# Kernel tuning notes

Hardware: AMD Instinct MI355X
Metric: run time of the kernel (lower is better)

## Reference

```python
import jax, jax.numpy as jnp
import numpy as np

SCALING = 32.0 / 16.0  # alpha / r

def setup_inputs() -> dict:
    key = jax.random.key(0)
    k1, k2, k3, k4 = jax.random.split(key, 4)
    B_, S, D_in, D_out, R = 4, 2048, 4096, 4096, 16
    x = jax.random.normal(k1, (B_, S, D_in), dtype=jnp.float32)
    W_base = jax.random.normal(k2, (D_out, D_in), dtype=jnp.float32) * 0.02
    b_base = jax.random.normal(k3, (D_out,), dtype=jnp.float32) * 0.02
    A = jax.random.normal(k4, (R, D_in), dtype=jnp.float32) * 0.02
    B = jnp.zeros((D_out, R), dtype=jnp.float32)  # lora_B init to zeros
    return {"x": x, "W_base": W_base, "b_base": b_base, "A": A, "B": B}

def reference(x, W_base, b_base, A, B):
    # base linear (stands in for dequantized 4-bit matmul): [B,S,Din] @ [Din,Dout]
    out = jnp.einsum('bsd,od->bso', x, W_base) + b_base
    # LoRA path: B(A(x)) * scaling, dropout=0 -> identity
    xa = jnp.einsum('bsd,rd->bsr', x, A)        # [B,S,r]
    delta = jnp.einsum('bsr,or->bso', xa, B)    # [B,S,Dout]
    return out + delta * SCALING
```

## Files before the change

### kernel.cpp

```cpp
#include <hip/hip_runtime.h>


typedef __attribute__((ext_vector_type(4))) float f32x4;
typedef __attribute__((ext_vector_type(8))) short bf16x8;

__device__ __forceinline__ unsigned short f2bf(float f) {
    unsigned u = __builtin_bit_cast(unsigned, f);
    unsigned r = u + 0x7fffu + ((u >> 16) & 1u);
    return (unsigned short)(r >> 16);
}

__device__ __forceinline__ void gload_lds16(const void* g, void* l) {
    __builtin_amdgcn_global_load_lds(
        (const __attribute__((address_space(1))) void*)g,
        (__attribute__((address_space(3))) void*)l, 16, 0, 0);
}

__global__ __launch_bounds__(256) void cast_x_kernel(
    const float* __restrict__ x, unsigned short* __restrict__ xb, int n8)
{
    int stride = gridDim.x * blockDim.x;
    for (int i = blockIdx.x * blockDim.x + threadIdx.x; i < n8; i += stride) {
        size_t base = (size_t)i * 8;
        float4 f0 = *(const float4*)&x[base];
        float4 f1 = *(const float4*)&x[base + 4];
        ushort4 o0, o1;
        o0.x = f2bf(f0.x); o0.y = f2bf(f0.y); o0.z = f2bf(f0.z); o0.w = f2bf(f0.w);
        o1.x = f2bf(f1.x); o1.y = f2bf(f1.y); o1.z = f2bf(f1.z); o1.w = f2bf(f1.w);
        *(ushort4*)&xb[base]     = o0;
        *(ushort4*)&xb[base + 4] = o1;
    }
}

__global__ __launch_bounds__(256) void prep_w_kernel(
    const float* __restrict__ W, const float* __restrict__ A,
    const float* __restrict__ Bl, unsigned short* __restrict__ wb,
    int K, float scale)
{
    __shared__ float Bs[16][16];
    const int t = threadIdx.x;
    const int n0 = blockIdx.y * 16;
    const int k0 = blockIdx.x * 256;
    {
        int nl = t >> 4, r = t & 15;
        Bs[nl][r] = Bl[(size_t)(n0 + nl) * 16 + r];
    }
    __syncthreads();

    const int lane = t & 63;
    const int wv = t >> 6;
    const int k = k0 + lane * 4;

    float4 av[16];
#pragma unroll
    for (int r = 0; r < 16; ++r)
        av[r] = *(const float4*)&A[(size_t)r * K + k];

#pragma unroll
    for (int j = 0; j < 4; ++j) {
        const int nl = wv * 4 + j;
        const int n = n0 + nl;
        float4 w = *(const float4*)&W[(size_t)n * K + k];
        float d0 = 0.f, d1 = 0.f, d2 = 0.f, d3 = 0.f;
#pragma unroll
        for (int r = 0; r < 16; ++r) {
            float b = Bs[nl][r];
            d0 += b * av[r].x; d1 += b * av[r].y;
            d2 += b * av[r].z; d3 += b * av[r].w;
        }
        ushort4 o;
        o.x = f2bf(w.x + scale * d0);
        o.y = f2bf(w.y + scale * d1);
        o.z = f2bf(w.z + scale * d2);
        o.w = f2bf(w.w + scale * d3);
        *(ushort4*)&wb[(size_t)n * K + k] = o;
    }
}


#define SETPRIO(p) __builtin_amdgcn_s_setprio(p)
#define BARRIER()  __builtin_amdgcn_s_barrier()
#define LGKM(n)    asm volatile("s_waitcnt lgkmcnt(" #n ")" ::: "memory")

__global__ __launch_bounds__(512, 2) void gemm256_kernel(
    const unsigned short* __restrict__ Xb, const unsigned short* __restrict__ Wb,
    const float* __restrict__ bias, float* __restrict__ out,
    int M, int N, int K)
{
    __shared__ __align__(16) unsigned short lds[2][2][2][8192];

    const int NT = K / 64;
    const int ntn = N / 256;
    int bid = blockIdx.x;
    {
        int per = gridDim.x >> 3;
        bid = (bid & 7) * per + (bid >> 3);
    }
    const int tm = bid / ntn, tn = bid % ntn;

    const int t = threadIdx.x;
    const int lane = t & 63, wave = t >> 6;
    const int wr = wave >> 2;
    const int wc = wave & 3;
    const int wch = wc >> 1;
    const int bro = (wc & 1) * 64;

    const int srow = t >> 3;
    const int scol = ((t & 7) * 8) ^ (((t >> 3) & 7) << 3);
    unsigned gA[2][2], gB[2][2];
#pragma unroll
    for (int h = 0; h < 2; ++h)
#pragma unroll
        for (int i = 0; i < 2; ++i) {
            gA[h][i] = (unsigned)((tm * 256 + h * 128 + i * 64 + srow) * K + scol);
            gB[h][i] = (unsigned)((tn * 256 + h * 128 + i * 64 + srow) * K + scol);
        }

#define ST_A4(buf, ktt)                                                         \
    _Pragma("unroll") for (int h = 0; h < 2; ++h)                               \
    _Pragma("unroll") for (int i = 0; i < 2; ++i)                               \
        gload_lds16(Xb + gA[h][i] + (ktt) * 64,                                 \
                    &lds[buf][0][h][i * 4096 + wave * 512]);
#define ST_B4(buf, ktt)                                                         \
    _Pragma("unroll") for (int h = 0; h < 2; ++h)                               \
    _Pragma("unroll") for (int i = 0; i < 2; ++i)                               \
        gload_lds16(Wb + gB[h][i] + (ktt) * 64,                                 \
                    &lds[buf][1][h][i * 4096 + wave * 512]);

    const int fr = lane & 15;
    const int hi16 = ((lane >> 4) & 3) * 16;
    const int bsw = (fr & 7) << 4;
    const int lo0 = hi16 ^ bsw;
    const int lo1 = (64 + hi16) ^ bsw;

    f32x4 acc[8][4] = {};
    bf16x8 a03[4][2], a47[4][2], b01[2][2], b23[2][2];

#define RD_A03(P)                                                               \
    _Pragma("unroll") for (int i = 0; i < 4; ++i) {                             \
        a03[i][0] = *(const bf16x8*)((P) + (i * 16 + fr) * 128 + lo0);          \
        a03[i][1] = *(const bf16x8*)((P) + (i * 16 + fr) * 128 + lo1);          \
    }
#define RD_A47(P)                                                               \
    _Pragma("unroll") for (int i = 0; i < 4; ++i) {                             \
        a47[i][0] = *(const bf16x8*)((P) + ((4 + i) * 16 + fr) * 128 + lo0);    \
        a47[i][1] = *(const bf16x8*)((P) + ((4 + i) * 16 + fr) * 128 + lo1);    \
    }
#define RD_B01(P)                                                               \
    _Pragma("unroll") for (int i = 0; i < 2; ++i) {                             \
        b01[i][0] = *(const bf16x8*)((P) + (bro + i * 16 + fr) * 128 + lo0);    \
        b01[i][1] = *(const bf16x8*)((P) + (bro + i * 16 + fr) * 128 + lo1);    \
    }
#define RD_B23(P)                                                               \
    _Pragma("unroll") for (int i = 0; i < 2; ++i) {                             \
        b23[i][0] = *(const bf16x8*)((P) + (bro + (2+i) * 16 + fr) * 128 + lo0);\
        b23[i][1] = *(const bf16x8*)((P) + (bro + (2+i) * 16 + fr) * 128 + lo1);\
    }

#define MFMA_Q(AV, BV, M0, N0)                                                  \
    _Pragma("unroll") for (int mi = 0; mi < 4; ++mi)                            \
    _Pragma("unroll") for (int ni = 0; ni < 2; ++ni)                            \
    _Pragma("unroll") for (int kk = 0; kk < 2; ++kk)                            \
        acc[(M0) + mi][(N0) + ni] = __builtin_amdgcn_mfma_f32_16x16x32_bf16(    \
            AV[mi][kk], BV[ni][kk], acc[(M0) + mi][(N0) + ni], 0, 0, 0);

    ST_A4(0, 0) ST_B4(0, 0)
    ST_A4(1, 1) ST_B4(1, 1)
    asm volatile("s_waitcnt vmcnt(8)" ::: "memory");
    BARRIER();
    {
        const char* pA = (const char*)&lds[0][0][wr][0];
        const char* pB = (const char*)&lds[0][1][wch][0];
        RD_A03(pA)
        RD_B01(pB)
    }

    for (int kt = 0; kt < NT; ++kt) {
        const int cur = kt & 1;
        const char* pA  = (const char*)&lds[cur][0][wr][0];
        const char* pB  = (const char*)&lds[cur][1][wch][0];
        const char* pA1 = (const char*)&lds[cur ^ 1][0][wr][0];
        const char* pB1 = (const char*)&lds[cur ^ 1][1][wch][0];

        RD_A47(pA)
        RD_B23(pB)

        LGKM(12);
        SETPRIO(1);
        MFMA_Q(a03, b01, 0, 0)
        SETPRIO(0);

        LGKM(4);
        SETPRIO(1);
        MFMA_Q(a47, b01, 4, 0)
        SETPRIO(0);

        LGKM(0);
        asm volatile("s_waitcnt vmcnt(0)" ::: "memory");
        BARRIER();

        if (kt + 2 < NT) { ST_A4(cur, kt + 2) ST_B4(cur, kt + 2) }

        SETPRIO(1);
        MFMA_Q(a03, b23, 0, 2)
        SETPRIO(0);

        if (kt + 1 < NT) { RD_B01(pB1) RD_A03(pA1) }

        SETPRIO(1);
        MFMA_Q(a47, b23, 4, 2)
        SETPRIO(0);
    }

    const int row0 = tm * 256 + wr * 128 + (lane >> 4) * 4;
    const int col0 = tn * 256 + wc * 64;
#pragma unroll
    for (int ni = 0; ni < 4; ++ni) {
        const int col = col0 + ni * 16 + fr;
        const float bv = bias[col];
#pragma unroll
        for (int mi = 0; mi < 8; ++mi) {
            const int row = row0 + mi * 16;
#pragma unroll
            for (int r = 0; r < 4; ++r)
                out[(size_t)(row + r) * N + col] = acc[mi][ni][r] + bv;
        }
    }
}

extern "C" void kernel_launch(void* const* d_in, const int* in_sizes, int n_in,
                              void* d_out, int out_size, void* d_ws, size_t ws_size,
                              hipStream_t stream)
{
    const float* x  = (const float*)d_in[0];
    const float* W  = (const float*)d_in[1];
    const float* b  = (const float*)d_in[2];
    const float* A  = (const float*)d_in[3];
    const float* Bl = (const float*)d_in[4];
    float* out = (float*)d_out;

    const int Dout = in_sizes[2];
    const int Din  = in_sizes[1] / Dout;
    const int M    = in_sizes[0] / Din;

    unsigned short* xb = (unsigned short*)d_ws;
    unsigned short* wb = xb + (size_t)M * Din;

    cast_x_kernel<<<2048, 256, 0, stream>>>(x, xb, M * Din / 8);

    dim3 gw(Din / 256, Dout / 16);
    prep_w_kernel<<<gw, 256, 0, stream>>>(W, A, Bl, wb, Din, 2.0f);

    const int grid = (M / 256) * (Dout / 256);
    gemm256_kernel<<<grid, 512, 0, stream>>>(xb, wb, b, out, M, Dout, Din);
}
```

Before: 301.9 us.

## Fuse prep kernels into one launch and re-stage GEMM k-loop phases

The x-to-bf16 cast and the LoRA-merged weight prep now run as one kernel launch, with the block index split between the two jobs. This removes a launch and lets the two memory-bound jobs overlap. The GEMM main loop is split into a templated per-k-tile routine, unrolled by two so buffer indices are compile-time. Its schedule changes to four phases, each with a full lgkmcnt wait and a barrier, and the global-to-LDS stores for A and B are spread across separate phases interleaved with LDS reads. The extra barriers and stricter waits may reduce latency hiding, and the loop now assumes an even number of k-tiles.

```diff
diff --git a/kernel.cpp b/kernel.cpp
--- a/kernel.cpp
+++ b/kernel.cpp
@@ -16,31 +16,31 @@
         (__attribute__((address_space(3))) void*)l, 16, 0, 0);
 }
 
-__global__ __launch_bounds__(256) void cast_x_kernel(
-    const float* __restrict__ x, unsigned short* __restrict__ xb, int n8)
-{
-    int stride = gridDim.x * blockDim.x;
-    for (int i = blockIdx.x * blockDim.x + threadIdx.x; i < n8; i += stride) {
-        size_t base = (size_t)i * 8;
-        float4 f0 = *(const float4*)&x[base];
-        float4 f1 = *(const float4*)&x[base + 4];
-        ushort4 o0, o1;
-        o0.x = f2bf(f0.x); o0.y = f2bf(f0.y); o0.z = f2bf(f0.z); o0.w = f2bf(f0.w);
-        o1.x = f2bf(f1.x); o1.y = f2bf(f1.y); o1.z = f2bf(f1.z); o1.w = f2bf(f1.w);
-        *(ushort4*)&xb[base]     = o0;
-        *(ushort4*)&xb[base + 4] = o1;
-    }
-}
-
-__global__ __launch_bounds__(256) void prep_w_kernel(
+__global__ __launch_bounds__(256) void prep_kernel(
+    const float* __restrict__ x, unsigned short* __restrict__ xb, int n8,
     const float* __restrict__ W, const float* __restrict__ A,
     const float* __restrict__ Bl, unsigned short* __restrict__ wb,
-    int K, float scale)
+    int K, float scale, int castBlocks)
 {
     __shared__ float Bs[16][16];
+    if ((int)blockIdx.x < castBlocks) {
+        int stride = castBlocks * 256;
+        for (int i = blockIdx.x * 256 + threadIdx.x; i < n8; i += stride) {
+            size_t base = (size_t)i * 8;
+            float4 f0 = *(const float4*)&x[base];
+            float4 f1 = *(const float4*)&x[base + 4];
+            ushort4 o0, o1;
+            o0.x = f2bf(f0.x); o0.y = f2bf(f0.y); o0.z = f2bf(f0.z); o0.w = f2bf(f0.w);
+            o1.x = f2bf(f1.x); o1.y = f2bf(f1.y); o1.z = f2bf(f1.z); o1.w = f2bf(f1.w);
+            *(ushort4*)&xb[base]     = o0;
+            *(ushort4*)&xb[base + 4] = o1;
+        }
+        return;
+    }
+    const int b = blockIdx.x - castBlocks;
     const int t = threadIdx.x;
-    const int n0 = blockIdx.y * 16;
-    const int k0 = blockIdx.x * 256;
+    const int n0 = (b >> 4) * 16;
+    const int k0 = (b & 15) * 256;
     {
         int nl = t >> 4, r = t & 15;
         Bs[nl][r] = Bl[(size_t)(n0 + nl) * 16 + r];
@@ -64,9 +64,9 @@
         float d0 = 0.f, d1 = 0.f, d2 = 0.f, d3 = 0.f;
 #pragma unroll
         for (int r = 0; r < 16; ++r) {
-            float b = Bs[nl][r];
-            d0 += b * av[r].x; d1 += b * av[r].y;
-            d2 += b * av[r].z; d3 += b * av[r].w;
+            float bb = Bs[nl][r];
+            d0 += bb * av[r].x; d1 += bb * av[r].y;
+            d2 += bb * av[r].z; d3 += bb * av[r].w;
         }
         ushort4 o;
         o.x = f2bf(w.x + scale * d0);
@@ -80,7 +80,101 @@
 
 #define SETPRIO(p) __builtin_amdgcn_s_setprio(p)
 #define BARRIER()  __builtin_amdgcn_s_barrier()
-#define LGKM(n)    asm volatile("s_waitcnt lgkmcnt(" #n ")" ::: "memory")
+#define LGKM0()    asm volatile("s_waitcnt lgkmcnt(0)" ::: "memory")
+
+typedef unsigned short lds_t[2][2][2][8192];
+
+struct GemmCtx {
+    const unsigned short* Xb;
+    const unsigned short* Wb;
+    unsigned gA[2][2], gB[2][2];
+    int wave, wr, wch, bro, fr, lo0, lo1;
+};
+
+#define ST_A4(buf, ktt)                                                         \
+    _Pragma("unroll") for (int h = 0; h < 2; ++h)                               \
+    _Pragma("unroll") for (int i = 0; i < 2; ++i)                               \
+        gload_lds16(c.Xb + c.gA[h][i] + (ktt) * 64,                             \
+                    &lds[buf][0][h][i * 4096 + c.wave * 512]);
+#define ST_B4(buf, ktt)                                                         \
+    _Pragma("unroll") for (int h = 0; h < 2; ++h)                               \
+    _Pragma("unroll") for (int i = 0; i < 2; ++i)                               \
+        gload_lds16(c.Wb + c.gB[h][i] + (ktt) * 64,                             \
+                    &lds[buf][1][h][i * 4096 + c.wave * 512]);
+
+#define RD_A03(P)                                                               \
+    _Pragma("unroll") for (int i = 0; i < 4; ++i) {                             \
+        a03[i][0] = *(const bf16x8*)((P) + (i * 16 + c.fr) * 128 + c.lo0);      \
+        a03[i][1] = *(const bf16x8*)((P) + (i * 16 + c.fr) * 128 + c.lo1);      \
+    }
+#define RD_A47(P)                                                               \
+    _Pragma("unroll") for (int i = 0; i < 4; ++i) {                             \
+        a47[i][0] = *(const bf16x8*)((P) + ((4 + i) * 16 + c.fr) * 128 + c.lo0);\
+        a47[i][1] = *(const bf16x8*)((P) + ((4 + i) * 16 + c.fr) * 128 + c.lo1);\
+    }
+#define RD_B01(P)                                                               \
+    _Pragma("unroll") for (int i = 0; i < 2; ++i) {                             \
+        b01[i][0] = *(const bf16x8*)((P) + (c.bro + i * 16 + c.fr) * 128 + c.lo0);\
+        b01[i][1] = *(const bf16x8*)((P) + (c.bro + i * 16 + c.fr) * 128 + c.lo1);\
+    }
+#define RD_B23(P)                                                               \
+    _Pragma("unroll") for (int i = 0; i < 2; ++i) {                             \
+        b23[i][0] = *(const bf16x8*)((P) + (c.bro + (2+i) * 16 + c.fr) * 128 + c.lo0);\
+        b23[i][1] = *(const bf16x8*)((P) + (c.bro + (2+i) * 16 + c.fr) * 128 + c.lo1);\
+    }
+
+#define MFMA_Q(AV, BV, M0, N0)                                                  \
+    _Pragma("unroll") for (int mi = 0; mi < 4; ++mi)                            \
+    _Pragma("unroll") for (int ni = 0; ni < 2; ++ni)                            \
+    _Pragma("unroll") for (int kk = 0; kk < 2; ++kk)                            \
+        acc[(M0) + mi][(N0) + ni] = __builtin_amdgcn_mfma_f32_16x16x32_bf16(    \
+            AV[mi][kk], BV[ni][kk], acc[(M0) + mi][(N0) + ni], 0, 0, 0);
+
+template<int CUR>
+__device__ __forceinline__ void ktile(
+    int kt, int NT, lds_t& lds, const GemmCtx& c,
+    f32x4 (&acc)[8][4],
+    bf16x8 (&a03)[4][2], bf16x8 (&a47)[4][2],
+    bf16x8 (&b01)[2][2], bf16x8 (&b23)[2][2])
+{
+    const char* pA  = (const char*)&lds[CUR][0][c.wr][0];
+    const char* pB  = (const char*)&lds[CUR][1][c.wch][0];
+    const char* pA1 = (const char*)&lds[CUR ^ 1][0][c.wr][0];
+    const char* pB1 = (const char*)&lds[CUR ^ 1][1][c.wch][0];
+    const bool stB = (kt + 1 < NT);
+    const bool stA = (kt + 2 < NT);
+
+    LGKM0();
+    RD_A47(pA)
+    SETPRIO(1);
+    MFMA_Q(a03, b01, 0, 0)
+    SETPRIO(0);
+    BARRIER();
+
+    LGKM0();
+    RD_B23(pB)
+    SETPRIO(1);
+    MFMA_Q(a47, b01, 4, 0)
+    SETPRIO(0);
+    asm volatile("s_waitcnt vmcnt(0)" ::: "memory");
+    BARRIER();
+
+    LGKM0();
+    if (stB) { RD_B01(pB1) }
+    if (stA) { ST_A4(CUR, kt + 2) }
+    SETPRIO(1);
+    MFMA_Q(a03, b23, 0, 2)
+    SETPRIO(0);
+    BARRIER();
+
+    LGKM0();
+    if (stB) { RD_A03(pA1) }
+    if (stA) { ST_B4(CUR, kt + 2) }
+    SETPRIO(1);
+    MFMA_Q(a47, b23, 4, 2)
+    SETPRIO(0);
+    BARRIER();
+}
 
 __global__ __launch_bounds__(512, 2) void gemm256_kernel(
     const unsigned short* __restrict__ Xb, const unsigned short* __restrict__ Wb,
@@ -99,124 +193,55 @@
     const int tm = bid / ntn, tn = bid % ntn;
 
     const int t = threadIdx.x;
-    const int lane = t & 63, wave = t >> 6;
-    const int wr = wave >> 2;
-    const int wc = wave & 3;
-    const int wch = wc >> 1;
-    const int bro = (wc & 1) * 64;
+    const int lane = t & 63;
+
+    GemmCtx c;
+    c.Xb = Xb; c.Wb = Wb;
+    c.wave = t >> 6;
+    c.wr  = c.wave >> 2;
+    const int wc = c.wave & 3;
+    c.wch = wc >> 1;
+    c.bro = (wc & 1) * 64;
+    c.fr  = lane & 15;
+    const int hi16 = ((lane >> 4) & 3) * 16;
+    const int bsw = (c.fr & 7) << 4;
+    c.lo0 = hi16 ^ bsw;
+    c.lo1 = (64 + hi16) ^ bsw;
 
     const int srow = t >> 3;
     const int scol = ((t & 7) * 8) ^ (((t >> 3) & 7) << 3);
-    unsigned gA[2][2], gB[2][2];
 #pragma unroll
     for (int h = 0; h < 2; ++h)
 #pragma unroll
         for (int i = 0; i < 2; ++i) {
-            gA[h][i] = (unsigned)((tm * 256 + h * 128 + i * 64 + srow) * K + scol);
-            gB[h][i] = (unsigned)((tn * 256 + h * 128 + i * 64 + srow) * K + scol);
-        }
-
-#define ST_A4(buf, ktt)                                                         \
-    _Pragma("unroll") for (int h = 0; h < 2; ++h)                               \
-    _Pragma("unroll") for (int i = 0; i < 2; ++i)                               \
-        gload_lds16(Xb + gA[h][i] + (ktt) * 64,                                 \
-                    &lds[buf][0][h][i * 4096 + wave * 512]);
-#define ST_B4(buf, ktt)                                                         \
-    _Pragma("unroll") for (int h = 0; h < 2; ++h)                               \
-    _Pragma("unroll") for (int i = 0; i < 2; ++i)                               \
-        gload_lds16(Wb + gB[h][i] + (ktt) * 64,                                 \
-                    &lds[buf][1][h][i * 4096 + wave * 512]);
-
-    const int fr = lane & 15;
-    const int hi16 = ((lane >> 4) & 3) * 16;
-    const int bsw = (fr & 7) << 4;
-    const int lo0 = hi16 ^ bsw;
-    const int lo1 = (64 + hi16) ^ bsw;
+            c.gA[h][i] = (unsigned)((tm * 256 + h * 128 + i * 64 + srow) * K + scol);
+            c.gB[h][i] = (unsigned)((tn * 256 + h * 128 + i * 64 + srow) * K + scol);
+        }
 
     f32x4 acc[8][4] = {};
     bf16x8 a03[4][2], a47[4][2], b01[2][2], b23[2][2];
-
-#define RD_A03(P)                                                               \
-    _Pragma("unroll") for (int i = 0; i < 4; ++i) {                             \
-        a03[i][0] = *(const bf16x8*)((P) + (i * 16 + fr) * 128 + lo0);          \
-        a03[i][1] = *(const bf16x8*)((P) + (i * 16 + fr) * 128 + lo1);          \
-    }
-#define RD_A47(P)                                                               \
-    _Pragma("unroll") for (int i = 0; i < 4; ++i) {                             \
-        a47[i][0] = *(const bf16x8*)((P) + ((4 + i) * 16 + fr) * 128 + lo0);    \
-        a47[i][1] = *(const bf16x8*)((P) + ((4 + i) * 16 + fr) * 128 + lo1);    \
-    }
-#define RD_B01(P)                                                               \
-    _Pragma("unroll") for (int i = 0; i < 2; ++i) {                             \
-        b01[i][0] = *(const bf16x8*)((P) + (bro + i * 16 + fr) * 128 + lo0);    \
-        b01[i][1] = *(const bf16x8*)((P) + (bro + i * 16 + fr) * 128 + lo1);    \
-    }
-#define RD_B23(P)                                                               \
-    _Pragma("unroll") for (int i = 0; i < 2; ++i) {                             \
-        b23[i][0] = *(const bf16x8*)((P) + (bro + (2+i) * 16 + fr) * 128 + lo0);\
-        b23[i][1] = *(const bf16x8*)((P) + (bro + (2+i) * 16 + fr) * 128 + lo1);\
-    }
-
-#define MFMA_Q(AV, BV, M0, N0)                                                  \
-    _Pragma("unroll") for (int mi = 0; mi < 4; ++mi)                            \
-    _Pragma("unroll") for (int ni = 0; ni < 2; ++ni)                            \
-    _Pragma("unroll") for (int kk = 0; kk < 2; ++kk)                            \
-        acc[(M0) + mi][(N0) + ni] = __builtin_amdgcn_mfma_f32_16x16x32_bf16(    \
-            AV[mi][kk], BV[ni][kk], acc[(M0) + mi][(N0) + ni], 0, 0, 0);
 
     ST_A4(0, 0) ST_B4(0, 0)
     ST_A4(1, 1) ST_B4(1, 1)
     asm volatile("s_waitcnt vmcnt(8)" ::: "memory");
     BARRIER();
     {
-        const char* pA = (const char*)&lds[0][0][wr][0];
-        const char* pB = (const char*)&lds[0][1][wch][0];
+        const char* pA = (const char*)&lds[0][0][c.wr][0];
+        const char* pB = (const char*)&lds[0][1][c.wch][0];
         RD_A03(pA)
         RD_B01(pB)
     }
 
-    for (int kt = 0; kt < NT; ++kt) {
-        const int cur = kt & 1;
-        const char* pA  = (const char*)&lds[cur][0][wr][0];
-        const char* pB  = (const char*)&lds[cur][1][wch][0];
-        const char* pA1 = (const char*)&lds[cur ^ 1][0][wr][0];
-        const char* pB1 = (const char*)&lds[cur ^ 1][1][wch][0];
-
-        RD_A47(pA)
-        RD_B23(pB)
-
-        LGKM(12);
-        SETPRIO(1);
-        MFMA_Q(a03, b01, 0, 0)
-        SETPRIO(0);
-
-        LGKM(4);
-        SETPRIO(1);
-        MFMA_Q(a47, b01, 4, 0)
-        SETPRIO(0);
-
-        LGKM(0);
-        asm volatile("s_waitcnt vmcnt(0)" ::: "memory");
-        BARRIER();
-
-        if (kt + 2 < NT) { ST_A4(cur, kt + 2) ST_B4(cur, kt + 2) }
-
-        SETPRIO(1);
-        MFMA_Q(a03, b23, 0, 2)
-        SETPRIO(0);
-
-        if (kt + 1 < NT) { RD_B01(pB1) RD_A03(pA1) }
-
-        SETPRIO(1);
-        MFMA_Q(a47, b23, 4, 2)
-        SETPRIO(0);
-    }
-
-    const int row0 = tm * 256 + wr * 128 + (lane >> 4) * 4;
+    for (int kt = 0; kt < NT; kt += 2) {
+        ktile<0>(kt,     NT, lds, c, acc, a03, a47, b01, b23);
+        ktile<1>(kt + 1, NT, lds, c, acc, a03, a47, b01, b23);
+    }
+
+    const int row0 = tm * 256 + c.wr * 128 + (lane >> 4) * 4;
     const int col0 = tn * 256 + wc * 64;
 #pragma unroll
     for (int ni = 0; ni < 4; ++ni) {
-        const int col = col0 + ni * 16 + fr;
+        const int col = col0 + ni * 16 + c.fr;
         const float bv = bias[col];
 #pragma unroll
         for (int mi = 0; mi < 8; ++mi) {
@@ -246,10 +271,10 @@
     unsigned short* xb = (unsigned short*)d_ws;
     unsigned short* wb = xb + (size_t)M * Din;
 
-    cast_x_kernel<<<2048, 256, 0, stream>>>(x, xb, M * Din / 8);
-
-    dim3 gw(Din / 256, Dout / 16);
-    prep_w_kernel<<<gw, 256, 0, stream>>>(W, A, Bl, wb, Din, 2.0f);
+    const int castBlocks = 2048;
+    const int prepBlocks = (Din / 256) * (Dout / 16);
+    prep_kernel<<<castBlocks + prepBlocks, 256, 0, stream>>>(
+        x, xb, M * Din / 8, W, A, Bl, wb, Din, 2.0f, castBlocks);
 
     const int grid = (M / 256) * (Dout / 256);
     gemm256_kernel<<<grid, 512, 0, stream>>>(xb, wb, b, out, M, Dout, Din);
```

After: 393.0 us. +30.2%, slower.

## Restructure GEMM main loop into four barrier-separated phases with split B/A staging

Applied to the files above, without the earlier changes.

Reorganizes the bf16 MFMA GEMM K-loop into four phases, each ending in a barrier. LDS reads for the next fragments are issued before each MFMA quadrant, and the global-to-LDS stores for tile kt+2 are split: B goes out in phase three and A in phase four. The vmcnt waits become finer-grained, so global loads can overlap the MFMA work instead of draining to zero once per iteration. The cost is four barriers per iteration instead of one, plus full lgkmcnt(0) waits that may serialize LDS reads with compute.

```diff
diff --git a/kernel.cpp b/kernel.cpp
--- a/kernel.cpp
+++ b/kernel.cpp
@@ -80,7 +80,8 @@
 
 #define SETPRIO(p) __builtin_amdgcn_s_setprio(p)
 #define BARRIER()  __builtin_amdgcn_s_barrier()
-#define LGKM(n)    asm volatile("s_waitcnt lgkmcnt(" #n ")" ::: "memory")
+#define LGKM0()    asm volatile("s_waitcnt lgkmcnt(0)" ::: "memory")
+#define VMCNT(n)   asm volatile("s_waitcnt vmcnt(" #n ")" ::: "memory")
 
 __global__ __launch_bounds__(512, 2) void gemm256_kernel(
     const unsigned short* __restrict__ Xb, const unsigned short* __restrict__ Wb,
@@ -164,9 +165,9 @@
         acc[(M0) + mi][(N0) + ni] = __builtin_amdgcn_mfma_f32_16x16x32_bf16(    \
             AV[mi][kk], BV[ni][kk], acc[(M0) + mi][(N0) + ni], 0, 0, 0);
 
-    ST_A4(0, 0) ST_B4(0, 0)
-    ST_A4(1, 1) ST_B4(1, 1)
-    asm volatile("s_waitcnt vmcnt(8)" ::: "memory");
+    ST_B4(0, 0) ST_A4(0, 0)
+    ST_B4(1, 1) ST_A4(1, 1)
+    VMCNT(8);
     BARRIER();
     {
         const char* pA = (const char*)&lds[0][0][wr][0];
@@ -181,35 +182,40 @@
         const char* pB  = (const char*)&lds[cur][1][wch][0];
         const char* pA1 = (const char*)&lds[cur ^ 1][0][wr][0];
         const char* pB1 = (const char*)&lds[cur ^ 1][1][wch][0];
-
+        const bool stB = (kt + 1 < NT);
+        const bool stA = (kt + 2 < NT);
+
+        LGKM0();
         RD_A47(pA)
+        SETPRIO(1);
+        MFMA_Q(a03, b01, 0, 0)
+        SETPRIO(0);
+        BARRIER();
+
+        LGKM0();
         RD_B23(pB)
-
-        LGKM(12);
-        SETPRIO(1);
-        MFMA_Q(a03, b01, 0, 0)
-        SETPRIO(0);
-
-        LGKM(4);
         SETPRIO(1);
         MFMA_Q(a47, b01, 4, 0)
         SETPRIO(0);
-
-        LGKM(0);
-        asm volatile("s_waitcnt vmcnt(0)" ::: "memory");
-        BARRIER();
-
-        if (kt + 2 < NT) { ST_A4(cur, kt + 2) ST_B4(cur, kt + 2) }
-
+        if (stB) { VMCNT(4); } else { VMCNT(0); }
+        BARRIER();
+
+        LGKM0();
+        if (stB) { RD_B01(pB1) }
+        if (stA) { ST_B4(cur, kt + 2) }
         SETPRIO(1);
         MFMA_Q(a03, b23, 0, 2)
         SETPRIO(0);
-
-        if (kt + 1 < NT) { RD_B01(pB1) RD_A03(pA1) }
-
+        if (stA) { VMCNT(4); } else { VMCNT(0); }
+        BARRIER();
+
+        LGKM0();
+        if (stB) { RD_A03(pA1) }
+        if (stA) { ST_A4(cur, kt + 2) }
         SETPRIO(1);
         MFMA_Q(a47, b23, 4, 2)
         SETPRIO(0);
+        BARRIER();
     }
 
     const int row0 = tm * 256 + wr * 128 + (lane >> 4) * 4;
```

New measurement: 303.4 us. Within noise of the previous version (+0.5%).
